# Kernel optimization log

Hardware: AMD Instinct MI355X
Metric: run time of the kernel (lower is better)

Reference implementation:

```python
import jax, jax.numpy as jnp
import numpy as np

B, N, C_IN, C_OUT, K = 16, 16384, 128, 128, 9


def setup_inputs() -> dict:
    key = jax.random.key(0)
    ks = jax.random.split(key, 7)
    x = jax.random.normal(ks[0], (B, N, C_IN), dtype=jnp.float32)
    indices = jax.random.randint(ks[1], (N, K), 0, N, dtype=jnp.int32)
    # P initialized near identity (as in the torch module) plus small noise
    P = jnp.eye(K, dtype=jnp.float32)[None].repeat(N, axis=0) \
        + 0.02 * jax.random.normal(ks[2], (N, K, K), dtype=jnp.float32)
    W_conv = jax.random.normal(ks[3], (C_OUT, K * C_IN), dtype=jnp.float32) * (1.0 / np.sqrt(K * C_IN))
    b_conv = jax.random.normal(ks[4], (C_OUT,), dtype=jnp.float32) * 0.01
    W_skip = jax.random.normal(ks[5], (C_OUT, C_IN), dtype=jnp.float32) * (1.0 / np.sqrt(C_IN))
    b_skip = jax.random.normal(ks[6], (C_OUT,), dtype=jnp.float32) * 0.01
    return {"x": x, "indices": indices, "P": P, "W_conv": W_conv,
            "b_conv": b_conv, "W_skip": W_skip, "b_skip": b_skip}


def reference(x, indices, P, W_conv, b_conv, W_skip, b_skip):
    b, n, c = x.shape
    k = P.shape[-1]
    # pad node axis with k zero rows (matches x_padded in torch module)
    x_pad = jnp.concatenate([x, jnp.zeros((b, k, c), dtype=x.dtype)], axis=1)
    # gather k neighbours per node: (b, n, k, c)
    nbr = jnp.take(x_pad, indices, axis=1)
    # per-node kxk permutation/mixing matmul: P (n,k,k) @ nbr (b,n,k,c)
    perm = jnp.einsum('nkj,bnjc->bnkc', P, nbr)
    flat = jax.nn.elu(perm.reshape(b, n, k * c))
    z = jax.nn.elu(jnp.einsum('bnf,of->bno', flat, W_conv) + b_conv)
    # skip connection
    z = jnp.einsum('bnc,oc->bno', x, W_skip) + b_skip + z
    return z
```

## Files before the change

### kernel.cpp

```cpp
#include <hip/hip_runtime.h>
#include <hip/hip_fp16.h>
#include <math.h>

#define B_ 16
#define N_ 16384
#define C_ 128
#define K_ 9
#define FCONV 1152
#define G_ 2
#define FPAD 1160
#define LDS_BYTES (G_ * B_ * FPAD * 2)

typedef _Float16 half8 __attribute__((ext_vector_type(8)));
typedef float floatx4 __attribute__((ext_vector_type(4)));

__device__ __forceinline__ float elu_f(float v) {
    return v > 0.f ? v : (__expf(v) - 1.f);
}

__global__ void build_wfrag(const float* __restrict__ Wc, const float* __restrict__ Ws,
                            _Float16* __restrict__ WcF, _Float16* __restrict__ WsF) {
    const int i = blockIdx.x * 256 + threadIdx.x;
    if (i < 8 * 36 * 64 * 8) {
        const int j = i & 7, lane = (i >> 3) & 63;
        const int rest = i >> 9;
        const int kc = rest % 36, ot = rest / 36;
        WcF[i] = (_Float16)Wc[(size_t)(ot * 16 + (lane & 15)) * FCONV + kc * 32 + (lane >> 4) * 8 + j];
    }
    if (i < 8 * 4 * 64 * 8) {
        const int j = i & 7, lane = (i >> 3) & 63;
        const int rest = i >> 9;
        const int kc = rest & 3, ot = rest >> 2;
        WsF[i] = (_Float16)Ws[(size_t)(ot * 16 + (lane & 15)) * C_ + kc * 32 + (lane >> 4) * 8 + j];
    }
}

template <bool WF16>
__global__ __launch_bounds__(256) void paiconv_mfma(
    const float* __restrict__ x,
    const int*   __restrict__ idx,
    const float* __restrict__ P,
    const void*  __restrict__ WcP,
    const float* __restrict__ bc,
    const void*  __restrict__ WsP,
    const float* __restrict__ bs,
    float*       __restrict__ out)
{
    extern __shared__ _Float16 flat_s[];
    __shared__ float P_s[G_ * 81];
    __shared__ int   idx_s[G_ * K_];

    const int tid = threadIdx.x;
    const int n0  = blockIdx.x * G_;

    if (tid < G_ * 81) {
        const int g = tid / 81, t = tid - g * 81;
        P_s[tid] = P[(size_t)(n0 + g) * 81 + t];
    }
    if (tid < G_ * K_) {
        const int g = tid / K_, j = tid - g * K_;
        idx_s[tid] = idx[(size_t)(n0 + g) * K_ + j];
    }
    __syncthreads();

    {
        const int c = tid & (C_ - 1);
        const int h = tid >> 7;
        for (int g = 0; g < G_; ++g) {
            int id[K_];
            #pragma unroll
            for (int j = 0; j < K_; ++j) id[j] = idx_s[g * K_ + j];
            const float* Pg = &P_s[g * 81];
            _Float16* fg = &flat_s[g * (B_ * FPAD)];

            float v[8][K_];
            #pragma unroll
            for (int i = 0; i < 8; ++i) {
                const int m = h * 8 + i;
                const float* xb = x + (size_t)m * (N_ * C_) + c;
                #pragma unroll
                for (int j = 0; j < K_; ++j)
                    v[i][j] = ((unsigned)id[j] < (unsigned)N_) ? xb[(size_t)id[j] * C_] : 0.f;
            }
            #pragma unroll
            for (int k = 0; k < K_; ++k) {
                float pr[K_];
                #pragma unroll
                for (int j = 0; j < K_; ++j) pr[j] = Pg[k * K_ + j];
                #pragma unroll
                for (int i = 0; i < 8; ++i) {
                    float s = 0.f;
                    #pragma unroll
                    for (int j = 0; j < K_; ++j) s = fmaf(pr[j], v[i][j], s);
                    fg[(h * 8 + i) * FPAD + k * C_ + c] = (_Float16)elu_f(s);
                }
            }
        }
    }
    __syncthreads();

    const int w    = tid >> 6;
    const int lane = tid & 63;
    const int col  = lane & 15;
    const int quad = lane >> 4;
    const int o0   = w * 32;

    floatx4 accC[G_][2], accS[G_][2];
    #pragma unroll
    for (int g = 0; g < G_; ++g)
        #pragma unroll
        for (int t = 0; t < 2; ++t) {
            accC[g][t] = (floatx4){0.f, 0.f, 0.f, 0.f};
            accS[g][t] = (floatx4){0.f, 0.f, 0.f, 0.f};
        }

    for (int k0 = 0; k0 < FCONV; k0 += 32) {
        half8 a[G_];
        #pragma unroll
        for (int g = 0; g < G_; ++g)
            a[g] = *(const half8*)&flat_s[g * (B_ * FPAD) + col * FPAD + k0 + quad * 8];
        #pragma unroll
        for (int t = 0; t < 2; ++t) {
            half8 b;
            if (WF16) {
                b = ((const half8*)WcP)[((w * 2 + t) * 36 + (k0 >> 5)) * 64 + lane];
            } else {
                const float* p = (const float*)WcP + (size_t)(o0 + t * 16 + col) * FCONV + k0 + quad * 8;
                const float4 w0 = *(const float4*)p;
                const float4 w1 = *(const float4*)(p + 4);
                b = (half8){(_Float16)w0.x, (_Float16)w0.y, (_Float16)w0.z, (_Float16)w0.w,
                            (_Float16)w1.x, (_Float16)w1.y, (_Float16)w1.z, (_Float16)w1.w};
            }
            #pragma unroll
            for (int g = 0; g < G_; ++g)
                accC[g][t] = __builtin_amdgcn_mfma_f32_16x16x32_f16(a[g], b, accC[g][t], 0, 0, 0);
        }
    }

    for (int k0 = 0; k0 < C_; k0 += 32) {
        half8 a[G_];
        #pragma unroll
        for (int g = 0; g < G_; ++g) {
            const float* p = x + (size_t)col * (N_ * C_) + (size_t)(n0 + g) * C_ + k0 + quad * 8;
            const float4 x0 = *(const float4*)p;
            const float4 x1 = *(const float4*)(p + 4);
            a[g] = (half8){(_Float16)x0.x, (_Float16)x0.y, (_Float16)x0.z, (_Float16)x0.w,
                           (_Float16)x1.x, (_Float16)x1.y, (_Float16)x1.z, (_Float16)x1.w};
        }
        #pragma unroll
        for (int t = 0; t < 2; ++t) {
            half8 b;
            if (WF16) {
                b = ((const half8*)WsP)[((w * 2 + t) * 4 + (k0 >> 5)) * 64 + lane];
            } else {
                const float* p = (const float*)WsP + (size_t)(o0 + t * 16 + col) * C_ + k0 + quad * 8;
                const float4 w0 = *(const float4*)p;
                const float4 w1 = *(const float4*)(p + 4);
                b = (half8){(_Float16)w0.x, (_Float16)w0.y, (_Float16)w0.z, (_Float16)w0.w,
                            (_Float16)w1.x, (_Float16)w1.y, (_Float16)w1.z, (_Float16)w1.w};
            }
            #pragma unroll
            for (int g = 0; g < G_; ++g)
                accS[g][t] = __builtin_amdgcn_mfma_f32_16x16x32_f16(a[g], b, accS[g][t], 0, 0, 0);
        }
    }

    float bcv[2], bsv[2];
    #pragma unroll
    for (int t = 0; t < 2; ++t) {
        bcv[t] = bc[o0 + t * 16 + col];
        bsv[t] = bs[o0 + t * 16 + col];
    }
    #pragma unroll
    for (int g = 0; g < G_; ++g) {
        const int n = n0 + g;
        #pragma unroll
        for (int t = 0; t < 2; ++t) {
            const int o = o0 + t * 16 + col;
            #pragma unroll
            for (int r = 0; r < 4; ++r) {
                const int m = quad * 4 + r;
                const float z = elu_f(accC[g][t][r] + bcv[t]);
                out[((size_t)m * N_ + n) * C_ + o] = z + accS[g][t][r] + bsv[t];
            }
        }
    }
}

extern "C" void kernel_launch(void* const* d_in, const int* in_sizes, int n_in,
                              void* d_out, int out_size, void* d_ws, size_t ws_size,
                              hipStream_t stream) {
    const float* x   = (const float*)d_in[0];
    const int*   idx = (const int*)  d_in[1];
    const float* P   = (const float*)d_in[2];
    const float* Wc  = (const float*)d_in[3];
    const float* bc  = (const float*)d_in[4];
    const float* Ws  = (const float*)d_in[5];
    const float* bs  = (const float*)d_in[6];
    float* out = (float*)d_out;

    const size_t wc_halfs = (size_t)8 * 36 * 64 * 8;
    const size_t ws_halfs = (size_t)8 * 4 * 64 * 8;
    const size_t need = (wc_halfs + ws_halfs) * sizeof(_Float16);

    if (ws_size >= need) {
        _Float16* WcF = (_Float16*)d_ws;
        _Float16* WsF = WcF + wc_halfs;
        build_wfrag<<<dim3(576), dim3(256), 0, stream>>>(Wc, Ws, WcF, WsF);
        hipFuncSetAttribute((const void*)paiconv_mfma<true>,
                            hipFuncAttributeMaxDynamicSharedMemorySize, LDS_BYTES);
        paiconv_mfma<true><<<dim3(N_ / G_), dim3(256), LDS_BYTES, stream>>>(
            x, idx, P, WcF, bc, WsF, bs, out);
    } else {
        hipFuncSetAttribute((const void*)paiconv_mfma<false>,
                            hipFuncAttributeMaxDynamicSharedMemorySize, LDS_BYTES);
        paiconv_mfma<false><<<dim3(N_ / G_), dim3(256), LDS_BYTES, stream>>>(
            x, idx, P, Wc, bc, Ws, bs, out);
    }
}
```

Before: 623.0 us.

## Pre-convert x to fp16 and process one node per block

Adds a pre-pass that converts all of x to fp16 in workspace, so the random neighbour gathers and the skip-path loads read half the bytes. Each block now handles one node instead of two, which halves LDS use, and launch bounds of 4 blocks per SIMD-group are requested for higher occupancy. The gather loop is split into two halves of four batch rows to reduce register pressure. The cost is an extra full pass over x (read fp32, write fp16) and the loss of weight-fragment reuse across two nodes per block.

Result: slower. 781.7 us (+25.5%).

```diff
diff --git a/kernel.cpp b/kernel.cpp
--- a/kernel.cpp
+++ b/kernel.cpp
@@ -7,15 +7,24 @@
 #define C_ 128
 #define K_ 9
 #define FCONV 1152
-#define G_ 2
 #define FPAD 1160
-#define LDS_BYTES (G_ * B_ * FPAD * 2)
+#define LDS_BYTES (B_ * FPAD * 2)
 
 typedef _Float16 half8 __attribute__((ext_vector_type(8)));
 typedef float floatx4 __attribute__((ext_vector_type(4)));
 
 __device__ __forceinline__ float elu_f(float v) {
     return v > 0.f ? v : (__expf(v) - 1.f);
+}
+
+__global__ __launch_bounds__(256) void convert_x(const float* __restrict__ x,
+                                                 _Float16* __restrict__ xh) {
+    const size_t i = ((size_t)blockIdx.x * 256 + threadIdx.x) * 8;
+    const float4 a = *(const float4*)(x + i);
+    const float4 b = *(const float4*)(x + i + 4);
+    half8 h = {(_Float16)a.x, (_Float16)a.y, (_Float16)a.z, (_Float16)a.w,
+               (_Float16)b.x, (_Float16)b.y, (_Float16)b.z, (_Float16)b.w};
+    *(half8*)(xh + i) = h;
 }
 
 __global__ void build_wfrag(const float* __restrict__ Wc, const float* __restrict__ Ws,
@@ -35,64 +44,65 @@
     }
 }
 
-template <bool WF16>
-__global__ __launch_bounds__(256) void paiconv_mfma(
-    const float* __restrict__ x,
-    const int*   __restrict__ idx,
-    const float* __restrict__ P,
-    const void*  __restrict__ WcP,
-    const float* __restrict__ bc,
-    const void*  __restrict__ WsP,
-    const float* __restrict__ bs,
-    float*       __restrict__ out)
+template <bool WF16, bool XH>
+__global__ __launch_bounds__(256, 4) void paiconv_mfma(
+    const float*    __restrict__ x,
+    const _Float16* __restrict__ xh,
+    const int*      __restrict__ idx,
+    const float*    __restrict__ P,
+    const void*     __restrict__ WcP,
+    const float*    __restrict__ bc,
+    const void*     __restrict__ WsP,
+    const float*    __restrict__ bs,
+    float*          __restrict__ out)
 {
     extern __shared__ _Float16 flat_s[];
-    __shared__ float P_s[G_ * 81];
-    __shared__ int   idx_s[G_ * K_];
+    __shared__ float P_s[81];
+    __shared__ int   idx_s[K_];
 
     const int tid = threadIdx.x;
-    const int n0  = blockIdx.x * G_;
-
-    if (tid < G_ * 81) {
-        const int g = tid / 81, t = tid - g * 81;
-        P_s[tid] = P[(size_t)(n0 + g) * 81 + t];
-    }
-    if (tid < G_ * K_) {
-        const int g = tid / K_, j = tid - g * K_;
-        idx_s[tid] = idx[(size_t)(n0 + g) * K_ + j];
-    }
+    const int n   = blockIdx.x;
+
+    if (tid < 81) P_s[tid] = P[(size_t)n * 81 + tid];
+    if (tid < K_) idx_s[tid] = idx[(size_t)n * K_ + tid];
     __syncthreads();
 
     {
         const int c = tid & (C_ - 1);
         const int h = tid >> 7;
-        for (int g = 0; g < G_; ++g) {
-            int id[K_];
+        int id[K_];
+        #pragma unroll
+        for (int j = 0; j < K_; ++j) id[j] = idx_s[j];
+
+        #pragma unroll
+        for (int q = 0; q < 2; ++q) {
+            float v[4][K_];
             #pragma unroll
-            for (int j = 0; j < K_; ++j) id[j] = idx_s[g * K_ + j];
-            const float* Pg = &P_s[g * 81];
-            _Float16* fg = &flat_s[g * (B_ * FPAD)];
-
-            float v[8][K_];
-            #pragma unroll
-            for (int i = 0; i < 8; ++i) {
-                const int m = h * 8 + i;
-                const float* xb = x + (size_t)m * (N_ * C_) + c;
-                #pragma unroll
-                for (int j = 0; j < K_; ++j)
-                    v[i][j] = ((unsigned)id[j] < (unsigned)N_) ? xb[(size_t)id[j] * C_] : 0.f;
+            for (int i = 0; i < 4; ++i) {
+                const int m = h * 8 + q * 4 + i;
+                if (XH) {
+                    const _Float16* xb = xh + (size_t)m * (N_ * C_) + c;
+                    #pragma unroll
+                    for (int j = 0; j < K_; ++j)
+                        v[i][j] = ((unsigned)id[j] < (unsigned)N_) ? (float)xb[(size_t)id[j] * C_] : 0.f;
+                } else {
+                    const float* xb = x + (size_t)m * (N_ * C_) + c;
+                    #pragma unroll
+                    for (int j = 0; j < K_; ++j)
+                        v[i][j] = ((unsigned)id[j] < (unsigned)N_) ? xb[(size_t)id[j] * C_] : 0.f;
+                }
             }
             #pragma unroll
             for (int k = 0; k < K_; ++k) {
                 float pr[K_];
                 #pragma unroll
-                for (int j = 0; j < K_; ++j) pr[j] = Pg[k * K_ + j];
+                for (int j = 0; j < K_; ++j) pr[j] = P_s[k * K_ + j];
                 #pragma unroll
-                for (int i = 0; i < 8; ++i) {
+                for (int i = 0; i < 4; ++i) {
                     float s = 0.f;
                     #pragma unroll
                     for (int j = 0; j < K_; ++j) s = fmaf(pr[j], v[i][j], s);
-                    fg[(h * 8 + i) * FPAD + k * C_ + c] = (_Float16)elu_f(s);
+                    flat_s[(h * 8 + q * 4 + i) * FPAD + k * C_ + c] = (_Float16)elu_f(s);
                 }
             }
         }
@@ -105,20 +115,15 @@
     const int quad = lane >> 4;
     const int o0   = w * 32;
 
-    floatx4 accC[G_][2], accS[G_][2];
+    floatx4 accC[2], accS[2];
     #pragma unroll
-    for (int g = 0; g < G_; ++g)
-        #pragma unroll
-        for (int t = 0; t < 2; ++t) {
-            accC[g][t] = (floatx4){0.f, 0.f, 0.f, 0.f};
-            accS[g][t] = (floatx4){0.f, 0.f, 0.f, 0.f};
-        }
+    for (int t = 0; t < 2; ++t) {
+        accC[t] = (floatx4){0.f, 0.f, 0.f, 0.f};
+        accS[t] = (floatx4){0.f, 0.f, 0.f, 0.f};
+    }
 
     for (int k0 = 0; k0 < FCONV; k0 += 32) {
-        half8 a[G_];
-        #pragma unroll
-        for (int g = 0; g < G_; ++g)
-            a[g] = *(const half8*)&flat_s[g * (B_ * FPAD) + col * FPAD + k0 + quad * 8];
+        const half8 a = *(const half8*)&flat_s[col * FPAD + k0 + quad * 8];
         #pragma unroll
         for (int t = 0; t < 2; ++t) {
             half8 b;
@@ -131,21 +136,20 @@
                 b = (half8){(_Float16)w0.x, (_Float16)w0.y, (_Float16)w0.z, (_Float16)w0.w,
                             (_Float16)w1.x, (_Float16)w1.y, (_Float16)w1.z, (_Float16)w1.w};
             }
-            #pragma unroll
-            for (int g = 0; g < G_; ++g)
-                accC[g][t] = __builtin_amdgcn_mfma_f32_16x16x32_f16(a[g], b, accC[g][t], 0, 0, 0);
+            accC[t] = __builtin_amdgcn_mfma_f32_16x16x32_f16(a, b, accC[t], 0, 0, 0);
         }
     }
 
     for (int k0 = 0; k0 < C_; k0 += 32) {
-        half8 a[G_];
-        #pragma unroll
-        for (int g = 0; g < G_; ++g) {
-            const float* p = x + (size_t)col * (N_ * C_) + (size_t)(n0 + g) * C_ + k0 + quad * 8;
+        half8 a;
+        if (XH) {
+            a = *(const half8*)(xh + (size_t)col * (N_ * C_) + (size_t)n * C_ + k0 + quad * 8);
+        } else {
+            const float* p = x + (size_t)col * (N_ * C_) + (size_t)n * C_ + k0 + quad * 8;
             const float4 x0 = *(const float4*)p;
             const float4 x1 = *(const float4*)(p + 4);
-            a[g] = (half8){(_Float16)x0.x, (_Float16)x0.y, (_Float16)x0.z, (_Float16)x0.w,
-                           (_Float16)x1.x, (_Float16)x1.y, (_Float16)x1.z, (_Float16)x1.w};
+            a = (half8){(_Float16)x0.x, (_Float16)x0.y, (_Float16)x0.z, (_Float16)x0.w,
+                        (_Float16)x1.x, (_Float16)x1.y, (_Float16)x1.z, (_Float16)x1.w};
         }
         #pragma unroll
         for (int t = 0; t < 2; ++t) {
@@ -159,30 +163,20 @@
                 b = (half8){(_Float16)w0.x, (_Float16)w0.y, (_Float16)w0.z, (_Float16)w0.w,
                             (_Float16)w1.x, (_Float16)w1.y, (_Float16)w1.z, (_Float16)w1.w};
             }
-            #pragma unroll
-            for (int g = 0; g < G_; ++g)
-                accS[g][t] = __builtin_amdgcn_mfma_f32_16x16x32_f16(a[g], b, accS[g][t], 0, 0, 0);
-        }
-    }
-
-    float bcv[2], bsv[2];
+            accS[t] = __builtin_amdgcn_mfma_f32_16x16x32_f16(a, b, accS[t], 0, 0, 0);
+        }
+    }
+
     #pragma unroll
     for (int t = 0; t < 2; ++t) {
-        bcv[t] = bc[o0 + t * 16 + col];
-        bsv[t] = bs[o0 + t * 16 + col];
-    }
-    #pragma unroll
-    for (int g = 0; g < G_; ++g) {
-        const int n = n0 + g;
-        #pragma unroll
-        for (int t = 0; t < 2; ++t) {
-            const int o = o0 + t * 16 + col;
-            #pragma unroll
-            for (int r = 0; r < 4; ++r) {
-                const int m = quad * 4 + r;
-                const float z = elu_f(accC[g][t][r] + bcv[t]);
-                out[((size_t)m * N_ + n) * C_ + o] = z + accS[g][t][r] + bsv[t];
-            }
+        const int o = o0 + t * 16 + col;
+        const float bcv = bc[o];
+        const float bsv = bs[o];
+        #pragma unroll
+        for (int r = 0; r < 4; ++r) {
+            const int m = quad * 4 + r;
+            const float z = elu_f(accC[t][r] + bcv);
+            out[((size_t)m * N_ + n) * C_ + o] = z + accS[t][r] + bsv;
         }
     }
 }
@@ -201,20 +195,32 @@
 
     const size_t wc_halfs = (size_t)8 * 36 * 64 * 8;
     const size_t ws_halfs = (size_t)8 * 4 * 64 * 8;
-    const size_t need = (wc_halfs + ws_halfs) * sizeof(_Float16);
-
-    if (ws_size >= need) {
+    const size_t xh_halfs = (size_t)B_ * N_ * C_;
+    const size_t need_w  = (wc_halfs + ws_halfs) * sizeof(_Float16);
+    const size_t need_wx = need_w + xh_halfs * sizeof(_Float16);
+
+    if (ws_size >= need_wx) {
+        _Float16* WcF = (_Float16*)d_ws;
+        _Float16* WsF = WcF + wc_halfs;
+        _Float16* xh  = WsF + ws_halfs;
+        build_wfrag<<<dim3(576), dim3(256), 0, stream>>>(Wc, Ws, WcF, WsF);
+        convert_x<<<dim3((int)(xh_halfs / 2048)), dim3(256), 0, stream>>>(x, xh);
+        hipFuncSetAttribute((const void*)paiconv_mfma<true, true>,
+                            hipFuncAttributeMaxDynamicSharedMemorySize, LDS_BYTES);
+        paiconv_mfma<true, true><<<dim3(N_), dim3(256), LDS_BYTES, stream>>>(
+            x, xh, idx, P, WcF, bc, WsF, bs, out);
+    } else if (ws_size >= need_w) {
         _Float16* WcF = (_Float16*)d_ws;
         _Float16* WsF = WcF + wc_halfs;
         build_wfrag<<<dim3(576), dim3(256), 0, stream>>>(Wc, Ws, WcF, WsF);
-        hipFuncSetAttribute((const void*)paiconv_mfma<true>,
+        hipFuncSetAttribute((const void*)paiconv_mfma<true, false>,
                             hipFuncAttributeMaxDynamicSharedMemorySize, LDS_BYTES);
-        paiconv_mfma<true><<<dim3(N_ / G_), dim3(256), LDS_BYTES, stream>>>(
-            x, idx, P, WcF, bc, WsF, bs, out);
+        paiconv_mfma<true, false><<<dim3(N_), dim3(256), LDS_BYTES, stream>>>(
+            x, nullptr, idx, P, WcF, bc, WsF, bs, out);
     } else {
-        hipFuncSetAttribute((const void*)paiconv_mfma<false>,
+        hipFuncSetAttribute((const void*)paiconv_mfma<false, false>,
                             hipFuncAttributeMaxDynamicSharedMemorySize, LDS_BYTES);
-        paiconv_mfma<false><<<dim3(N_ / G_), dim3(256), LDS_BYTES, stream>>>(
-            x, idx, P, Wc, bc, Ws, bs, out);
-    }
-}
+        paiconv_mfma<false, false><<<dim3(N_), dim3(256), LDS_BYTES, stream>>>(
+            x, nullptr, idx, P, Wc, bc, Ws, bs, out);
+    }
+}
```
